# Performance work log

Hardware: AMD Instinct MI355X
Metric: run time of the kernel (lower is better)

The kernel has to match this reference:

```python
import jax, jax.numpy as jnp
import numpy as np

N = 50000      # nodes
E = 800000     # edges (before self loops)
H = 4          # heads
C = 32         # hidden_channels per head
HC = H * C     # 128
L = 3          # num_layers - 2 conv blocks
G = 128        # graphs in batch
OUT = 10       # out_channels
VOCAB = 100
EPS = 1e-5


def setup_inputs() -> dict:
    key = jax.random.key(0)
    ks = jax.random.split(key, 16)
    s = 0.1
    return {
        "x_idx": jax.random.randint(ks[0], (N,), 0, VOCAB),
        "edge_index": jax.random.randint(ks[1], (2, E), 0, N),
        "batch": jnp.sort(jax.random.randint(ks[2], (N,), 0, G)),
        "embed": jax.random.normal(ks[3], (VOCAB, HC), jnp.float32) * s,
        "bn_gamma": jnp.ones((L, HC), jnp.float32),
        "bn_beta": jnp.zeros((L, HC), jnp.float32),
        "lin_W": jax.random.normal(ks[4], (L, C, HC), jnp.float32) * s,   # maps HC -> C (hidden)
        "lin_b": jnp.zeros((L, C), jnp.float32),
        "gat_W": jax.random.normal(ks[5], (L, HC, C), jnp.float32) * s,   # maps C -> H*C
        "att_src": jax.random.normal(ks[6], (L, H, C), jnp.float32) * s,
        "att_dst": jax.random.normal(ks[7], (L, H, C), jnp.float32) * s,
        "gat_b": jnp.zeros((L, HC), jnp.float32),
        "readout_W": jax.random.normal(ks[8], (OUT, HC), jnp.float32) * s,
        "readout_b": jnp.zeros((OUT,), jnp.float32),
    }


def _segment_softmax(logits, seg, num_segments):
    # logits: [E, H], seg: [E]
    m = jax.ops.segment_max(logits, seg, num_segments=num_segments)
    m = jnp.where(jnp.isfinite(m), m, 0.0)
    e = jnp.exp(logits - m[seg])
    z = jax.ops.segment_sum(e, seg, num_segments=num_segments)
    return e / (z[seg] + 1e-16)


def _forward(x_idx, edge_index, batch, embed, bn_gamma, bn_beta, lin_W, lin_b,
             gat_W, att_src, att_dst, gat_b, readout_W, readout_b):
    x = embed[x_idx]                                   # [N, HC]
    loops = jnp.arange(N)
    src = jnp.concatenate([edge_index[0], loops])      # add_self_loops=True
    dst = jnp.concatenate([edge_index[1], loops])
    for l in range(L):
        # BatchNorm1d (batch statistics)
        mean = jnp.mean(x, axis=0)
        var = jnp.var(x, axis=0)
        x = bn_gamma[l] * (x - mean) * jax.lax.rsqrt(var + EPS) + bn_beta[l]
        # Linear(HC -> C) + relu; dropout = identity (eval)
        x = jax.nn.relu(x @ lin_W[l].T + lin_b[l])      # [N, C]
        # GATConv(C -> C, heads=H, concat)
        h = (x @ gat_W[l].T).reshape(N, H, C)           # [N, H, C]
        a_src = jnp.sum(h * att_src[l], axis=-1)        # [N, H]
        a_dst = jnp.sum(h * att_dst[l], axis=-1)        # [N, H]
        logits = jax.nn.leaky_relu(a_src[src] + a_dst[dst], 0.2)  # [E+N, H]
        alpha = _segment_softmax(logits, dst, N)        # softmax over in-edges of each dst
        msg = h[src] * alpha[:, :, None]                # [E+N, H, C]
        x = jax.ops.segment_sum(msg, dst, num_segments=N).reshape(N, HC) + gat_b[l]
    x = x @ readout_W.T + readout_b                     # [N, OUT]
    return jax.ops.segment_sum(x, batch, num_segments=G)  # [G, OUT]


def reference(x_idx, edge_index, batch, embed, bn_gamma, bn_beta, lin_W, lin_b,
              gat_W, att_src, att_dst, gat_b, readout_W, readout_b):
    return _forward(x_idx, edge_index, batch, embed, bn_gamma, bn_beta, lin_W, lin_b,
                    gat_W, att_src, att_dst, gat_b, readout_W, readout_b)
```

## Files before the change

kernel.cpp:

```cpp
#include <hip/hip_runtime.h>

constexpr int NN   = 50000;
constexpr int NE   = 800000;
constexpr int NHD  = 4;
constexpr int CC   = 32;
constexpr int HCC  = 128;
constexpr int NL   = 3;
constexpr int NG   = 128;
constexpr int NOUT = 10;
constexpr float BN_EPS = 1e-5f;

constexpr int X2S = 67;
constexpr int YS = 33;
constexpr int NSLOT = 64;
constexpr int NBUK = (NN + 127) / 128;
constexpr int EB  = 2048;
constexpr int EMB_BLKS = 512;


typedef __attribute__((ext_vector_type(2))) float f32x2;

__device__ inline unsigned f2bf_pack(float a, float b) {
    unsigned ua = __float_as_uint(a); ua += 0x7FFFu + ((ua >> 16) & 1u);
    unsigned ub = __float_as_uint(b); ub += 0x7FFFu + ((ub >> 16) & 1u);
    return (ua >> 16) | (ub & 0xFFFF0000u);
}
__device__ inline float bf_lo(unsigned p) { return __uint_as_float(p << 16); }
__device__ inline float bf_hi(unsigned p) { return __uint_as_float(p & 0xFFFF0000u); }
__device__ inline f32x2 bfpair(unsigned p) {
    f32x2 r; r.x = __uint_as_float(p << 16); r.y = __uint_as_float(p & 0xFFFF0000u);
    return r;
}

__global__ __launch_bounds__(256) void k_pre(const int* __restrict__ idx,
                                             const float* __restrict__ embed,
                                             unsigned* __restrict__ xp,
                                             float* __restrict__ stats,
                                             const int* __restrict__ ei,
                                             int* __restrict__ bkcnt,
                                             const int* __restrict__ batch,
                                             float* __restrict__ gcnt) {
    int tid = threadIdx.x;
    if (blockIdx.x < EMB_BLKS) {
        __shared__ float A[256], B[256], C[256], D[256];
        int i0 = blockIdx.x * 256 + tid;
        int stride = EMB_BLKS * 256;
        float s0 = 0.f, s1 = 0.f, q0 = 0.f, q1 = 0.f;
        for (int i = i0; i < NN * 64; i += stride) {
            int n = i >> 6, c2 = (i & 63) << 1;
            float2 ev = *(const float2*)(embed + (size_t)idx[n] * HCC + c2);
            xp[i] = f2bf_pack(ev.x, ev.y);
            s0 += ev.x; q0 += ev.x * ev.x;
            s1 += ev.y; q1 += ev.y * ev.y;
        }
        A[tid] = s0; B[tid] = s1; C[tid] = q0; D[tid] = q1;
        __syncthreads();
        int slot = blockIdx.x & (NSLOT - 1);
        if (tid < 64) {
            int p = tid;
            float S0 = A[p] + A[p + 64] + A[p + 128] + A[p + 192];
            float S1 = B[p] + B[p + 64] + B[p + 128] + B[p + 192];
            float Q0 = C[p] + C[p + 64] + C[p + 128] + C[p + 192];
            float Q1 = D[p] + D[p + 64] + D[p + 128] + D[p + 192];
            atomicAdd(&stats[slot * 256 + 2 * p],           S0);
            atomicAdd(&stats[slot * 256 + 2 * p + 1],       S1);
            atomicAdd(&stats[slot * 256 + HCC + 2 * p],     Q0);
            atomicAdd(&stats[slot * 256 + HCC + 2 * p + 1], Q1);
        }
    } else {
        __shared__ int hist[NBUK];
        __shared__ int lgc[NG];
        int b = blockIdx.x - EMB_BLKS;
        int e0 = b * EB, nE = min(EB, NE - e0);
        for (int i = tid; i < NBUK; i += 256) hist[i] = 0;
        for (int i = tid; i < NG; i += 256) lgc[i] = 0;
        __syncthreads();
        for (int i = tid; i < nE; i += 256)
            atomicAdd(&hist[ei[NE + e0 + i] >> 7], 1);
        int n0 = b * 128;
        if (tid < 128) {
            int n = n0 + tid;
            if (n < NN) atomicAdd(&lgc[batch[n]], 1);
        }
        __syncthreads();
        for (int i = tid; i < NBUK; i += 256)
            if (hist[i]) atomicAdd(&bkcnt[i], hist[i]);
        for (int i = tid; i < NG; i += 256)
            if (lgc[i]) atomicAdd(&gcnt[i], (float)lgc[i]);
    }
}

__global__ __launch_bounds__(512) void k_bscan(const int* __restrict__ bkcnt,
                                               int* __restrict__ bbase,
                                               int* __restrict__ bcnt,
                                               int* __restrict__ rowptr) {
    __shared__ int sc[512];
    int t = threadIdx.x;
    int v = (t < NBUK) ? bkcnt[t] : 0;
    sc[t] = v;
    __syncthreads();
#pragma unroll
    for (int off = 1; off < 512; off <<= 1) {
        int u = (t >= off) ? sc[t - off] : 0;
        __syncthreads();
        sc[t] += u;
        __syncthreads();
    }
    if (t < NBUK) {
        int excl = sc[t] - v;
        bbase[t] = excl;
        bcnt[t]  = excl;
    }
    if (t == 0) rowptr[NN] = NE;
}

__global__ __launch_bounds__(256) void k_bin(const int* __restrict__ ei,
                                             int* __restrict__ bcnt,
                                             unsigned* __restrict__ e_src) {
    __shared__ int hist[NBUK], base[NBUK];
    int b = blockIdx.x, t = threadIdx.x;
    int e0 = b * EB;
    int nE = min(EB, NE - e0);

    for (int i = t; i < NBUK; i += 256) hist[i] = 0;
    __syncthreads();
    for (int i = t; i < nE; i += 256)
        atomicAdd(&hist[ei[NE + e0 + i] >> 7], 1);
    __syncthreads();
    for (int i = t; i < NBUK; i += 256) {
        int c = hist[i];
        if (c) base[i] = atomicAdd(&bcnt[i], c);
        hist[i] = 0;
    }
    __syncthreads();
    for (int i = t; i < nE; i += 256) {
        int e = e0 + i;
        int d = ei[NE + e];
        int s = ei[e];
        int bk = d >> 7;
        int pos = base[bk] + atomicAdd(&hist[bk], 1);
        e_src[pos] = (unsigned)s | ((unsigned)(d & 127) << 17);
    }
}

__global__ __launch_bounds__(512) void k_place(const int* __restrict__ bbase,
                                               unsigned* __restrict__ e_src,
                                               int* __restrict__ rowptr) {
    __shared__ int lcnt[128], sc[128], lrp[128], cnt[128];
    int b = blockIdx.x, t = threadIdx.x;
    int d0 = b * 128;
    int rS = bbase[b];
    int rE = (b + 1 < NBUK) ? bbase[b + 1] : NE;
    int n = rE - rS;
    if (t < 128) { lcnt[t] = 0; cnt[t] = 0; }
    __syncthreads();
    unsigned pk[7];
#pragma unroll
    for (int k = 0; k < 7; k++) {
        int i = t + k * 512;
        if (i < n) {
            pk[k] = e_src[rS + i];
            atomicAdd(&lcnt[pk[k] >> 17], 1);
        }
    }
    __syncthreads();
    if (t < 128) sc[t] = lcnt[t];
    __syncthreads();
#pragma unroll
    for (int off = 1; off < 128; off <<= 1) {
        int u = (t < 128 && t >= off) ? sc[t - off] : 0;
        __syncthreads();
        if (t < 128) sc[t] += u;
        __syncthreads();
    }
    if (t < 128) {
        int start = rS + sc[t] - lcnt[t];
        lrp[t] = start;
        int d = d0 + t;
        if (d < NN) rowptr[d] = start;
    }
    __syncthreads();
#pragma unroll
    for (int k = 0; k < 7; k++) {
        int i = t + k * 512;
        if (i < n) {
            unsigned p = pk[k];
            int dl = p >> 17;
            int pos = lrp[dl] + atomicAdd(&cnt[dl], 1);
            e_src[pos] = p & 0x1FFFFu;
        }
    }
}

__global__ __launch_bounds__(256) void k_fused(const unsigned* __restrict__ xp,
                                               const float* __restrict__ stats,
                                               const float* __restrict__ gamma,
                                               const float* __restrict__ beta,
                                               const float* __restrict__ W1,
                                               const float* __restrict__ b1,
                                               const float* __restrict__ W2,
                                               const float* __restrict__ aS,
                                               const float* __restrict__ aD,
                                               unsigned* __restrict__ h,
                                               float* __restrict__ asrc,
                                               float* __restrict__ adst) {
    __shared__ unsigned xb2[64 * X2S];
    __shared__ float yt[64 * YS];
    __shared__ float __attribute__((aligned(16))) ssl[256];
    int tid = threadIdx.x;
    int node0 = blockIdx.x * 64;
    int nNodes = min(64, NN - node0);

    {
        float s = 0.f;
        for (int sl = 0; sl < NSLOT; sl++) s += stats[sl * 256 + tid];
        yt[tid] = s;
    }
    __syncthreads();
    if (tid < 128) {
        float S = yt[tid], Q = yt[128 + tid];
        float mean = S * (1.0f / NN);
        float var  = Q * (1.0f / NN) - mean * mean;
        float sc   = gamma[tid] * rsqrtf(var + BN_EPS);
        ssl[tid]       = sc;
        ssl[HCC + tid] = beta[tid] - mean * sc;
    }
    __syncthreads();

    {
        for (int q4 = tid; q4 < nNodes * 16; q4 += 256) {
            int n = q4 >> 4, c8 = q4 & 15;
            uint4 xv = *(const uint4*)(xp + (size_t)(node0 + n) * 64 + c8 * 4);
            int c = c8 * 8;
            float4 sc0 = *(const float4*)&ssl[c];
            float4 sc1 = *(const float4*)&ssl[c + 4];
            float4 sh0 = *(const float4*)&ssl[HCC + c];
            float4 sh1 = *(const float4*)&ssl[HCC + c + 4];
            unsigned* dst = &xb2[n * X2S + c8 * 4];
            dst[0] = f2bf_pack(bf_lo(xv.x) * sc0.x + sh0.x, bf_hi(xv.x) * sc0.y + sh0.y);
            dst[1] = f2bf_pack(bf_lo(xv.y) * sc0.z + sh0.z, bf_hi(xv.y) * sc0.w + sh0.w);
            dst[2] = f2bf_pack(bf_lo(xv.z) * sc1.x + sh1.x, bf_hi(xv.z) * sc1.y + sh1.y);
            dst[3] = f2bf_pack(bf_lo(xv.w) * sc1.z + sh1.z, bf_hi(xv.w) * sc1.w + sh1.w);
        }
    }
    __syncthreads();

    int lane = tid & 63;
    int wv = __builtin_amdgcn_readfirstlane(tid >> 6);
    int n = lane;

    {
        int j0 = wv * 8;
        const float* w1p = W1 + j0 * 128;
        float acc[8];
#pragma unroll
        for (int k = 0; k < 8; k++) acc[k] = b1[j0 + k];
        if (n < nNodes) {
            for (int cb = 0; cb < 128; cb += 4) {
                unsigned p0 = xb2[n * X2S + (cb >> 1)];
                unsigned p1 = xb2[n * X2S + (cb >> 1) + 1];
                float xv0 = bf_lo(p0), xv1 = bf_hi(p0);
                float xv2 = bf_lo(p1), xv3 = bf_hi(p1);
#pragma unroll
                for (int k = 0; k < 8; k++) {
                    float4 w = *(const float4*)&w1p[k * 128 + cb];
                    acc[k] += xv0 * w.x + xv1 * w.y + xv2 * w.z + xv3 * w.w;
                }
            }
#pragma unroll
            for (int k = 0; k < 8; k++) yt[n * YS + j0 + k] = fmaxf(acc[k], 0.f);
        }
    }
    __syncthreads();

    if (n < nNodes) {
        int k0 = wv * 32, hd = wv;
        const float* w2p = W2 + k0 * 32;
        const float* aSp = aS + hd * 32;
        const float* aDp = aD + hd * 32;
        float yreg[32];
#pragma unroll
        for (int j = 0; j < 32; j++) yreg[j] = yt[n * YS + j];
        float sa = 0.f, da = 0.f;
        unsigned* hrow = h + (size_t)(node0 + n) * 64;
        for (int kb = 0; kb < 32; kb += 8) {
            float acck[8];
#pragma unroll
            for (int kk = 0; kk < 8; kk++) acck[kk] = 0.f;
#pragma unroll
            for (int j = 0; j < 32; j += 4) {
#pragma unroll
                for (int kk = 0; kk < 8; kk++) {
                    float4 w = *(const float4*)&w2p[(kb + kk) * 32 + j];
                    acck[kk] += yreg[j] * w.x + yreg[j + 1] * w.y +
                                yreg[j + 2] * w.z + yreg[j + 3] * w.w;
                }
            }
#pragma unroll
            for (int kk = 0; kk < 8; kk++) {
                sa += acck[kk] * aSp[kb + kk];
                da += acck[kk] * aDp[kb + kk];
            }
            uint4 pk;
            pk.x = f2bf_pack(acck[0], acck[1]);
            pk.y = f2bf_pack(acck[2], acck[3]);
            pk.z = f2bf_pack(acck[4], acck[5]);
            pk.w = f2bf_pack(acck[6], acck[7]);
            *(uint4*)(hrow + ((kb) >> 1) + (k0 >> 1)) = pk;
        }
        asrc[(node0 + n) * 4 + hd] = sa;
        adst[(node0 + n) * 4 + hd] = da;
    }
}

__global__ __launch_bounds__(256) void k_agg(const int* __restrict__ rowptr,
                                             const int* __restrict__ e_src,
                                             const float* __restrict__ asrc,
                                             const float* __restrict__ adst,
                                             const unsigned* __restrict__ h,
                                             const float* __restrict__ gat_b,
                                             unsigned* __restrict__ xo,
                                             float* __restrict__ stats,
                                             const int* __restrict__ batch,
                                             float* __restrict__ gsum,
                                             int mode) {
    int tid = threadIdx.x, lane = tid & 63, wv = tid >> 6;
    int g  = lane >> 4;
    int li = lane & 15;
    int hd = li >> 2;
    int d  = blockIdx.x * 16 + wv * 4 + g;

    float4 bA = *(const float4*)(gat_b + li * 8);
    float4 bB = *(const float4*)(gat_b + li * 8 + 4);

    int begin = rowptr[d];
    int end   = rowptr[d + 1];
    float adv = adst[d * 4 + hd];
    float asl = asrc[d * 4 + hd];
    uint4 hs  = *(const uint4*)(h + (size_t)d * 64 + li * 4);

    f32x2 acc0 = {0.f, 0.f}, acc1 = {0.f, 0.f}, acc2 = {0.f, 0.f}, acc3 = {0.f, 0.f};
    float ws = 0.f;

    int s[4];
    if (begin < end) {
#pragma unroll
        for (int t = 0; t < 4; t++) s[t] = e_src[min(begin + t, end - 1)];
    }

    for (int j = begin; j < end; j += 4) {
        uint4 hv[4];
#pragma unroll
        for (int t = 0; t < 4; t++) hv[t] = *(const uint4*)(h + (size_t)s[t] * 64 + li * 4);
        float av[4];
#pragma unroll
        for (int t = 0; t < 4; t++) av[t] = asrc[s[t] * 4 + hd];
        int jn = j + 4;
        int sn[4];
#pragma unroll
        for (int t = 0; t < 4; t++) sn[t] = s[t];
        if (jn < end) {
#pragma unroll
            for (int t = 0; t < 4; t++) sn[t] = e_src[min(jn + t, end - 1)];
        }
#pragma unroll
        for (int t = 0; t < 4; t++) {
            float l = av[t] + adv; l = l > 0.f ? l : 0.2f * l;
            float w = (j + t < end) ? __expf(l) : 0.f;
            f32x2 w2; w2.x = w; w2.y = w;
            acc0 += w2 * bfpair(hv[t].x);
            acc1 += w2 * bfpair(hv[t].y);
            acc2 += w2 * bfpair(hv[t].z);
            acc3 += w2 * bfpair(hv[t].w);
            ws += w;
        }
#pragma unroll
        for (int t = 0; t < 4; t++) s[t] = sn[t];
    }

    {
        float l = asl + adv; l = l > 0.f ? l : 0.2f * l;
        float w = __expf(l);
        f32x2 w2; w2.x = w; w2.y = w;
        acc0 += w2 * bfpair(hs.x);
        acc1 += w2 * bfpair(hs.y);
        acc2 += w2 * bfpair(hs.z);
        acc3 += w2 * bfpair(hs.w);
        ws += w;
    }

    float inv = 1.0f / (ws + 1e-16f);
    float o[8];
    o[0] = acc0.x * inv + bA.x; o[1] = acc0.y * inv + bA.y;
    o[2] = acc1.x * inv + bA.z; o[3] = acc1.y * inv + bA.w;
    o[4] = acc2.x * inv + bB.x; o[5] = acc2.y * inv + bB.y;
    o[6] = acc3.x * inv + bB.z; o[7] = acc3.y * inv + bB.w;

    __shared__ float redS[16 * 128], redQ[16 * 128];
    __shared__ int bg[16];
    int r = wv * 4 + g;

    if (mode == 1) {
        uint4 pk;
        pk.x = f2bf_pack(o[0], o[1]);
        pk.y = f2bf_pack(o[2], o[3]);
        pk.z = f2bf_pack(o[4], o[5]);
        pk.w = f2bf_pack(o[6], o[7]);
        *(uint4*)(xo + (size_t)d * 64 + li * 4) = pk;

#pragma unroll
        for (int k = 0; k < 8; k++) {
            redS[r * 128 + li * 8 + k] = o[k];
            redQ[r * 128 + li * 8 + k] = o[k] * o[k];
        }
        __syncthreads();
        int slot = blockIdx.x & (NSLOT - 1);
        if (tid < 128) {
            float v = 0.f;
#pragma unroll
            for (int rr = 0; rr < 16; rr++) v += redS[rr * 128 + tid];
            atomicAdd(&stats[slot * 256 + tid], v);
        } else {
            int c = tid - 128;
            float v = 0.f;
#pragma unroll
            for (int rr = 0; rr < 16; rr++) v += redQ[rr * 128 + c];
            atomicAdd(&stats[slot * 256 + HCC + c], v);
        }
    } else {
        if (li == 0) bg[r] = batch[d];
#pragma unroll
        for (int k = 0; k < 8; k++) redS[r * 128 + li * 8 + k] = o[k];
        __syncthreads();
        if (tid < 128) {
            float sacc = 0.f;
            int curg = bg[0];
#pragma unroll
            for (int rr = 0; rr < 16; rr++) {
                int gg = bg[rr];
                if (gg != curg) {
                    atomicAdd(&gsum[curg * HCC + tid], sacc);
                    sacc = 0.f; curg = gg;
                }
                sacc += redS[rr * 128 + tid];
            }
            atomicAdd(&gsum[curg * HCC + tid], sacc);
        }
    }
}

__global__ __launch_bounds__(128) void k_out(const float* __restrict__ gsum,
                                             const float* __restrict__ gcnt,
                                             const float* __restrict__ W,
                                             const float* __restrict__ bb,
                                             float* __restrict__ out) {
    __shared__ float v[128];
    int g = blockIdx.x, t = threadIdx.x;
    v[t] = gsum[g * HCC + t];
    __syncthreads();
    if (t < NOUT) {
        float acc = gcnt[g] * bb[t];
        const float* wr = W + t * HCC;
        for (int c = 0; c < HCC; c++) acc += v[c] * wr[c];
        out[g * NOUT + t] = acc;
    }
}

extern "C" void kernel_launch(void* const* d_in, const int* in_sizes, int n_in,
                              void* d_out, int out_size, void* d_ws, size_t ws_size,
                              hipStream_t stream) {
    const int*   x_idx = (const int*)d_in[0];
    const int*   ei    = (const int*)d_in[1];
    const int*   batch = (const int*)d_in[2];
    const float* embed = (const float*)d_in[3];
    const float* bn_g  = (const float*)d_in[4];
    const float* bn_b  = (const float*)d_in[5];
    const float* lin_W = (const float*)d_in[6];
    const float* lin_b = (const float*)d_in[7];
    const float* gat_W = (const float*)d_in[8];
    const float* att_s = (const float*)d_in[9];
    const float* att_d = (const float*)d_in[10];
    const float* gat_b = (const float*)d_in[11];
    const float* ro_W  = (const float*)d_in[12];
    const float* ro_b  = (const float*)d_in[13];
    float* out = (float*)d_out;

    const size_t STG = (size_t)NSLOT * 256;
    unsigned* xp    = (unsigned*)d_ws;
    unsigned* h     = xp + (size_t)NN * 64;
    float*    asrc  = (float*)(h + (size_t)NN * 64);
    float*    adst  = asrc + (size_t)NN * NHD;
    float*    stats = adst + (size_t)NN * NHD;
    float*    gsum  = stats + 3 * STG;
    float*    gcnt  = gsum + (size_t)NG * HCC;
    int*      bkcnt  = (int*)(gcnt + NG);
    int*      bbase  = bkcnt + NBUK;
    int*      bcnt   = bbase + NBUK;
    int*      rowptr = bcnt + NBUK;
    unsigned* e_src  = (unsigned*)(rowptr + NN + 1);

    hipMemsetAsync(stats, 0,
                   (3 * STG + (size_t)NG * HCC + NG) * sizeof(float) + NBUK * sizeof(int),
                   stream);

    k_pre<<<EMB_BLKS + (NE + EB - 1) / EB, 256, 0, stream>>>(x_idx, embed, xp, stats,
                                                             ei, bkcnt, batch, gcnt);
    k_bscan<<<1, 512, 0, stream>>>(bkcnt, bbase, bcnt, rowptr);
    k_bin<<<(NE + EB - 1) / EB, 256, 0, stream>>>(ei, bcnt, e_src);
    k_place<<<NBUK, 512, 0, stream>>>(bbase, e_src, rowptr);

    for (int l = 0; l < NL; ++l) {
        k_fused<<<(NN + 63) / 64, 256, 0, stream>>>(xp, stats + l * STG,
                                                    bn_g + l * HCC, bn_b + l * HCC,
                                                    lin_W + l * CC * HCC, lin_b + l * CC,
                                                    gat_W + l * HCC * CC,
                                                    att_s + l * NHD * CC,
                                                    att_d + l * NHD * CC,
                                                    h, asrc, adst);
        k_agg<<<NN / 16, 256, 0, stream>>>(rowptr, (const int*)e_src, asrc, adst, h,
                                           gat_b + l * HCC, xp,
                                           stats + (l + 1) * STG,
                                           batch, gsum,
                                           (l < NL - 1) ? 1 : 2);
    }

    k_out<<<NG, 128, 0, stream>>>(gsum, gcnt, ro_W, ro_b, out);
}
```

Measured before the change: 334.5 us.

## Double k_fused block to 512 threads and share per-edge exp via shuffles in k_agg

k_fused now runs 8 waves per 64-node block. The work is split finer: each wave computes 4 linear outputs instead of 8, and half a head (16 channels) of the GAT projection. Partial attention dot products are reduced through shared memory, and the BN stat reduction is split across two halves. In k_agg, each lane computes the exp for only one of the four edges in a batch and broadcasts it with __shfl, which replaces 4 redundant asrc loads and exps per lane. The cost is an extra barrier, more shared memory, and shuffle instructions.

```diff
diff --git a/kernel.cpp b/kernel.cpp
--- a/kernel.cpp
+++ b/kernel.cpp
@@ -192,7 +192,7 @@
     }
 }
 
-__global__ __launch_bounds__(256) void k_fused(const unsigned* __restrict__ xp,
+__global__ __launch_bounds__(512) void k_fused(const unsigned* __restrict__ xp,
                                                const float* __restrict__ stats,
                                                const float* __restrict__ gamma,
                                                const float* __restrict__ beta,
@@ -207,18 +207,21 @@
     __shared__ unsigned xb2[64 * X2S];
     __shared__ float yt[64 * YS];
     __shared__ float __attribute__((aligned(16))) ssl[256];
+    __shared__ float sdS[8][64], sdD[8][64];
     int tid = threadIdx.x;
     int node0 = blockIdx.x * 64;
     int nNodes = min(64, NN - node0);
 
     {
+        int col = tid & 255, half = tid >> 8;
         float s = 0.f;
-        for (int sl = 0; sl < NSLOT; sl++) s += stats[sl * 256 + tid];
+        for (int sl = half * 32; sl < half * 32 + 32; sl++) s += stats[sl * 256 + col];
         yt[tid] = s;
     }
     __syncthreads();
     if (tid < 128) {
-        float S = yt[tid], Q = yt[128 + tid];
+        float S = yt[tid] + yt[256 + tid];
+        float Q = yt[128 + tid] + yt[384 + tid];
         float mean = S * (1.0f / NN);
         float var  = Q * (1.0f / NN) - mean * mean;
         float sc   = gamma[tid] * rsqrtf(var + BN_EPS);
@@ -227,21 +230,19 @@
     }
     __syncthreads();
 
-    {
-        for (int q4 = tid; q4 < nNodes * 16; q4 += 256) {
-            int n = q4 >> 4, c8 = q4 & 15;
-            uint4 xv = *(const uint4*)(xp + (size_t)(node0 + n) * 64 + c8 * 4);
-            int c = c8 * 8;
-            float4 sc0 = *(const float4*)&ssl[c];
-            float4 sc1 = *(const float4*)&ssl[c + 4];
-            float4 sh0 = *(const float4*)&ssl[HCC + c];
-            float4 sh1 = *(const float4*)&ssl[HCC + c + 4];
-            unsigned* dst = &xb2[n * X2S + c8 * 4];
-            dst[0] = f2bf_pack(bf_lo(xv.x) * sc0.x + sh0.x, bf_hi(xv.x) * sc0.y + sh0.y);
-            dst[1] = f2bf_pack(bf_lo(xv.y) * sc0.z + sh0.z, bf_hi(xv.y) * sc0.w + sh0.w);
-            dst[2] = f2bf_pack(bf_lo(xv.z) * sc1.x + sh1.x, bf_hi(xv.z) * sc1.y + sh1.y);
-            dst[3] = f2bf_pack(bf_lo(xv.w) * sc1.z + sh1.z, bf_hi(xv.w) * sc1.w + sh1.w);
-        }
+    for (int q4 = tid; q4 < nNodes * 16; q4 += 512) {
+        int n = q4 >> 4, c8 = q4 & 15;
+        uint4 xv = *(const uint4*)(xp + (size_t)(node0 + n) * 64 + c8 * 4);
+        int c = c8 * 8;
+        float4 sc0 = *(const float4*)&ssl[c];
+        float4 sc1 = *(const float4*)&ssl[c + 4];
+        float4 sh0 = *(const float4*)&ssl[HCC + c];
+        float4 sh1 = *(const float4*)&ssl[HCC + c + 4];
+        unsigned* dst = &xb2[n * X2S + c8 * 4];
+        dst[0] = f2bf_pack(bf_lo(xv.x) * sc0.x + sh0.x, bf_hi(xv.x) * sc0.y + sh0.y);
+        dst[1] = f2bf_pack(bf_lo(xv.y) * sc0.z + sh0.z, bf_hi(xv.y) * sc0.w + sh0.w);
+        dst[2] = f2bf_pack(bf_lo(xv.z) * sc1.x + sh1.x, bf_hi(xv.z) * sc1.y + sh1.y);
+        dst[3] = f2bf_pack(bf_lo(xv.w) * sc1.z + sh1.z, bf_hi(xv.w) * sc1.w + sh1.w);
     }
     __syncthreads();
 
@@ -250,11 +251,11 @@
     int n = lane;
 
     {
-        int j0 = wv * 8;
+        int j0 = wv * 4;
         const float* w1p = W1 + j0 * 128;
-        float acc[8];
-#pragma unroll
-        for (int k = 0; k < 8; k++) acc[k] = b1[j0 + k];
+        float acc[4];
+#pragma unroll
+        for (int k = 0; k < 4; k++) acc[k] = b1[j0 + k];
         if (n < nNodes) {
             for (int cb = 0; cb < 128; cb += 4) {
                 unsigned p0 = xb2[n * X2S + (cb >> 1)];
@@ -262,54 +263,63 @@
                 float xv0 = bf_lo(p0), xv1 = bf_hi(p0);
                 float xv2 = bf_lo(p1), xv3 = bf_hi(p1);
 #pragma unroll
-                for (int k = 0; k < 8; k++) {
+                for (int k = 0; k < 4; k++) {
                     float4 w = *(const float4*)&w1p[k * 128 + cb];
                     acc[k] += xv0 * w.x + xv1 * w.y + xv2 * w.z + xv3 * w.w;
                 }
             }
 #pragma unroll
-            for (int k = 0; k < 8; k++) yt[n * YS + j0 + k] = fmaxf(acc[k], 0.f);
-        }
-    }
-    __syncthreads();
-
-    if (n < nNodes) {
-        int k0 = wv * 32, hd = wv;
-        const float* w2p = W2 + k0 * 32;
-        const float* aSp = aS + hd * 32;
-        const float* aDp = aD + hd * 32;
-        float yreg[32];
-#pragma unroll
-        for (int j = 0; j < 32; j++) yreg[j] = yt[n * YS + j];
-        float sa = 0.f, da = 0.f;
-        unsigned* hrow = h + (size_t)(node0 + n) * 64;
-        for (int kb = 0; kb < 32; kb += 8) {
-            float acck[8];
-#pragma unroll
-            for (int kk = 0; kk < 8; kk++) acck[kk] = 0.f;
-#pragma unroll
-            for (int j = 0; j < 32; j += 4) {
+            for (int k = 0; k < 4; k++) yt[n * YS + j0 + k] = fmaxf(acc[k], 0.f);
+        }
+    }
+    __syncthreads();
+
+    {
+        int hd = wv >> 1, hh = wv & 1;
+        int c0 = hd * 32 + hh * 16;
+        const float* w2p = W2 + c0 * 32;
+        const float* aSp = aS + c0;
+        const float* aDp = aD + c0;
+        if (n < nNodes) {
+            float yreg[32];
+#pragma unroll
+            for (int j = 0; j < 32; j++) yreg[j] = yt[n * YS + j];
+            float sa = 0.f, da = 0.f;
+            unsigned* hrow = h + (size_t)(node0 + n) * 64;
+            for (int kb = 0; kb < 16; kb += 8) {
+                float acck[8];
+#pragma unroll
+                for (int kk = 0; kk < 8; kk++) acck[kk] = 0.f;
+#pragma unroll
+                for (int j = 0; j < 32; j += 4) {
+#pragma unroll
+                    for (int kk = 0; kk < 8; kk++) {
+                        float4 w = *(const float4*)&w2p[(kb + kk) * 32 + j];
+                        acck[kk] += yreg[j] * w.x + yreg[j + 1] * w.y +
+                                    yreg[j + 2] * w.z + yreg[j + 3] * w.w;
+                    }
+                }
 #pragma unroll
                 for (int kk = 0; kk < 8; kk++) {
-                    float4 w = *(const float4*)&w2p[(kb + kk) * 32 + j];
-                    acck[kk] += yreg[j] * w.x + yreg[j + 1] * w.y +
-                                yreg[j + 2] * w.z + yreg[j + 3] * w.w;
+                    sa += acck[kk] * aSp[kb + kk];
+                    da += acck[kk] * aDp[kb + kk];
                 }
+                uint4 pk;
+                pk.x = f2bf_pack(acck[0], acck[1]);
+                pk.y = f2bf_pack(acck[2], acck[3]);
+                pk.z = f2bf_pack(acck[4], acck[5]);
+                pk.w = f2bf_pack(acck[6], acck[7]);
+                *(uint4*)(hrow + ((c0 + kb) >> 1)) = pk;
             }
-#pragma unroll
-            for (int kk = 0; kk < 8; kk++) {
-                sa += acck[kk] * aSp[kb + kk];
-                da += acck[kk] * aDp[kb + kk];
-            }
-            uint4 pk;
-            pk.x = f2bf_pack(acck[0], acck[1]);
-            pk.y = f2bf_pack(acck[2], acck[3]);
-            pk.z = f2bf_pack(acck[4], acck[5]);
-            pk.w = f2bf_pack(acck[6], acck[7]);
-            *(uint4*)(hrow + ((kb) >> 1) + (k0 >> 1)) = pk;
-        }
-        asrc[(node0 + n) * 4 + hd] = sa;
-        adst[(node0 + n) * 4 + hd] = da;
+            sdS[wv][n] = sa;
+            sdD[wv][n] = da;
+        }
+    }
+    __syncthreads();
+    if ((wv & 1) == 0 && n < nNodes) {
+        int hd = wv >> 1;
+        asrc[(node0 + n) * 4 + hd] = sdS[wv][n] + sdS[wv + 1][n];
+        adst[(node0 + n) * 4 + hd] = sdD[wv][n] + sdD[wv + 1][n];
     }
 }
 
@@ -328,7 +338,9 @@
     int g  = lane >> 4;
     int li = lane & 15;
     int hd = li >> 2;
+    int te = li & 3;
     int d  = blockIdx.x * 16 + wv * 4 + g;
+    int gbase = lane & 48;
 
     float4 bA = *(const float4*)(gat_b + li * 8);
     float4 bB = *(const float4*)(gat_b + li * 8 + 4);
@@ -352,9 +364,7 @@
         uint4 hv[4];
 #pragma unroll
         for (int t = 0; t < 4; t++) hv[t] = *(const uint4*)(h + (size_t)s[t] * 64 + li * 4);
-        float av[4];
-#pragma unroll
-        for (int t = 0; t < 4; t++) av[t] = asrc[s[t] * 4 + hd];
+        float avme = asrc[s[te] * 4 + hd];
         int jn = j + 4;
         int sn[4];
 #pragma unroll
@@ -363,10 +373,12 @@
 #pragma unroll
             for (int t = 0; t < 4; t++) sn[t] = e_src[min(jn + t, end - 1)];
         }
+        float lme = avme + adv; lme = lme > 0.f ? lme : 0.2f * lme;
+        float wme = __expf(lme);
 #pragma unroll
         for (int t = 0; t < 4; t++) {
-            float l = av[t] + adv; l = l > 0.f ? l : 0.2f * l;
-            float w = (j + t < end) ? __expf(l) : 0.f;
+            float wt = __shfl(wme, gbase + (hd << 2) + t, 64);
+            float w = (j + t < end) ? wt : 0.f;
             f32x2 w2; w2.x = w; w2.y = w;
             acc0 += w2 * bfpair(hv[t].x);
             acc1 += w2 * bfpair(hv[t].y);
@@ -510,7 +522,7 @@
     k_place<<<NBUK, 512, 0, stream>>>(bbase, e_src, rowptr);
 
     for (int l = 0; l < NL; ++l) {
-        k_fused<<<(NN + 63) / 64, 256, 0, stream>>>(xp, stats + l * STG,
+        k_fused<<<(NN + 63) / 64, 512, 0, stream>>>(xp, stats + l * STG,
                                                     bn_g + l * HCC, bn_b + l * HCC,
                                                     lin_W + l * CC * HCC, lin_b + l * CC,
                                                     gat_W + l * HCC * CC,
```

Measured after the change: 372.3 us. 11.3% more time.
